# Performance work log

Hardware: AMD Instinct MI355X
Metric: run time of the kernel (lower is better)

The kernel has to match this reference:

```python
import jax, jax.numpy as jnp
import numpy as np

FG_THRESH = 0.5   # cfg.TRAIN.FG_THRESH
BG_THRESH = 0.1   # cfg.TRAIN.BG_THRESH
EPS = 1e-9
N_STREAMS = 4

def _area(b):
    return (b[..., 2] - b[..., 0] + 1.0) * (b[..., 3] - b[..., 1] + 1.0)

def _pairwise_iou(bb, gt):
    # bb [R,4], gt [G,4] -> [R,G] pascal IoU (with +1)
    x1 = jnp.maximum(bb[:, None, 0], gt[None, :, 0])
    y1 = jnp.maximum(bb[:, None, 1], gt[None, :, 1])
    x2 = jnp.minimum(bb[:, None, 2], gt[None, :, 2])
    y2 = jnp.minimum(bb[:, None, 3], gt[None, :, 3])
    iw = jnp.maximum(x2 - x1 + 1.0, 0.0)
    ih = jnp.maximum(y2 - y1 + 1.0, 0.0)
    inter = iw * ih
    return inter / (_area(bb)[:, None] + _area(gt)[None, :] - inter)

def _iou_vs_one(boxes, bm):
    # boxes [4,4] vs single box bm [4] -> mutual iou [4]
    x1 = jnp.maximum(boxes[:, 0], bm[0])
    y1 = jnp.maximum(boxes[:, 1], bm[1])
    x2 = jnp.minimum(boxes[:, 2], bm[2])
    y2 = jnp.minimum(boxes[:, 3], bm[3])
    iw = jnp.maximum(x2 - x1 + 1.0, 0.0)
    ih = jnp.maximum(y2 - y1 + 1.0, 0.0)
    inter = iw * ih
    return inter / (_area(boxes) + _area(bm) - inter)

def _select_per_class(boxes, present):
    # boxes [4,4] top proposals of the 4 streams for one class; present: bool
    # Faithful port of the instance_selector while-loop (at most 4 iterations).
    area = _area(boxes)
    active = jnp.full((N_STREAMS,), present)
    selected = jnp.zeros((N_STREAMS,), bool)
    idx = jnp.arange(N_STREAMS)
    for _ in range(N_STREAMS):
        m = jnp.argmax(jnp.where(active, area, -jnp.inf))
        bm = boxes[m]
        iou = _iou_vs_one(boxes, bm)
        enclosed = ((boxes[:, 0] > bm[0]) & (boxes[:, 1] > bm[1]) &
                    (boxes[:, 2] < bm[2]) & (boxes[:, 3] < bm[3]))
        pick = active & (idx == m)                      # max-area pick
        keep = active & (iou < 0.1) & (~enclosed)        # kept as extra gt
        selected = selected | pick | keep
        # removed: high-overlap (>0.3, includes m itself), enclosed, kept
        active = active & ~((iou > 0.3) | enclosed | keep)
    return selected

def instance_selector(cls_probs, rois, im_labels):
    # cls_probs [4,R,C], rois [R,4], im_labels [1,C]
    top_idx = jnp.argmax(cls_probs, axis=1)                      # [4,C]
    top_boxes = rois[top_idx]                                    # [4,C,4]
    top_scores = jnp.take_along_axis(cls_probs, top_idx[:, None, :], axis=1)[:, 0, :]  # [4,C]
    boxes_c = jnp.transpose(top_boxes, (1, 0, 2))                # [C,4,4]
    scores_c = top_scores.T                                      # [C,4]
    present = im_labels[0] > 0                                   # [C]
    selected = jax.vmap(_select_per_class)(boxes_c, present)     # [C,4]
    C = scores_c.shape[0]
    gt_boxes = boxes_c.reshape(-1, 4)                            # [4C,4]
    gt_scores = scores_c.reshape(-1)                             # [4C]
    gt_classes = jnp.repeat(jnp.arange(1, C + 1), N_STREAMS)     # [4C]
    return gt_boxes, gt_classes, gt_scores, selected.reshape(-1)

def pcl_loss(rois, cls_prob_new, gt_boxes, gt_classes, gt_scores, valid):
    R = rois.shape[0]
    G = gt_boxes.shape[0]
    ov = _pairwise_iou(rois, gt_boxes)                   # [R,G]
    ov = jnp.where(valid[None, :], ov, -1.0)             # mask unselected gts
    assign = jnp.argmax(ov, axis=1)
    maxov = jnp.max(ov, axis=1)
    lab = gt_classes[assign]
    w = gt_scores[assign]
    bg = maxov < FG_THRESH
    lab = jnp.where(bg, 0, lab)
    assign = jnp.where(bg, -1, assign)
    w = jnp.where(maxov < BG_THRESH, 0.0, w)
    p = jnp.clip(cls_prob_new, EPS, 1.0 - EPS)
    prob_a = p[jnp.arange(R), lab]                       # prob at assigned class
    fg = (assign >= 0).astype(p.dtype)
    seg = jnp.where(assign >= 0, assign, G)              # dummy bucket G
    sums = jax.ops.segment_sum(prob_a * fg, seg, num_segments=G + 1)[:G]
    counts = jax.ops.segment_sum(fg, seg, num_segments=G + 1)[:G]
    mean_prob = sums / jnp.maximum(counts, 1.0)
    mean_safe = jnp.where(counts > 0, mean_prob, 1.0)
    pos = -jnp.sum(jnp.where(valid & (counts > 0),
                             jnp.log(mean_safe) * counts * gt_scores, 0.0))
    n_mask = jnp.where(lab == 0, w, 0.0)
    neg = -jnp.sum(jnp.log(p[:, 0]) * n_mask)
    return (pos + neg) / max(800, R)

def setup_inputs() -> dict:
    key = jax.random.key(0)
    ks = jax.random.split(key, 10)
    R, C, W, H = 100000, 20, 1000.0, 1000.0
    cx = jax.random.uniform(ks[0], (R,)) * (W - 100.0) + 50.0
    cy = jax.random.uniform(ks[1], (R,)) * (H - 100.0) + 50.0
    bw = jax.random.uniform(ks[2], (R,)) * 400.0 + 16.0
    bh = jax.random.uniform(ks[3], (R,)) * 400.0 + 16.0
    x1 = jnp.clip(cx - bw / 2, 0.0, W - 2.0)
    y1 = jnp.clip(cy - bh / 2, 0.0, H - 2.0)
    x2 = jnp.maximum(jnp.minimum(cx + bw / 2, W - 1.0), x1 + 1.0)
    y2 = jnp.maximum(jnp.minimum(cy + bh / 2, H - 1.0), y1 + 1.0)
    rois = jnp.stack([x1, y1, x2, y2], axis=1).astype(jnp.float32)
    cls0 = jax.random.uniform(ks[4], (R, C), dtype=jnp.float32)
    cls1 = jax.random.uniform(ks[5], (R, C), dtype=jnp.float32)
    cls2 = jax.random.uniform(ks[6], (R, C), dtype=jnp.float32)
    cls3 = jax.random.uniform(ks[7], (R, C), dtype=jnp.float32)
    cls_prob_new = jax.nn.softmax(jax.random.normal(ks[8], (R, C + 1), dtype=jnp.float32), axis=1)
    im_labels = (jax.random.uniform(ks[9], (1, C)) < 0.15).astype(jnp.int32)
    im_labels = im_labels.at[0, 0].set(1)  # ensure at least one positive class
    return {"rois": rois, "cls0_prob": cls0, "cls1_prob": cls1,
            "cls2_prob": cls2, "cls3_prob": cls3,
            "cls_prob_new": cls_prob_new, "im_labels": im_labels}

def reference(rois, cls0_prob, cls1_prob, cls2_prob, cls3_prob, cls_prob_new, im_labels):
    cls_probs = jnp.stack([cls0_prob, cls1_prob, cls2_prob, cls3_prob])  # [4,R,C]
    gtb, gtc, gts, valid = instance_selector(cls_probs, rois, im_labels)
    loss = pcl_loss(rois, cls_prob_new, gtb, gtc, gts, valid)
    return loss, gtb, gts, valid
```

## Files before the change

kernel.cpp:

```cpp
#include <hip/hip_runtime.h>
#include <cfloat>
#include <climits>
#include <math.h>

#define NSTREAM 4
#define NCLS    20
#define NGT     (NSTREAM * NCLS)
#define NBLK    128
#define TPB     256

__global__ __launch_bounds__(TPB) void top_argmax_kernel(
    const float* __restrict__ c0, const float* __restrict__ c1,
    const float* __restrict__ c2, const float* __restrict__ c3,
    float* __restrict__ pv, int* __restrict__ pi, int R)
{
    const float* cls = (blockIdx.y == 0) ? c0 : (blockIdx.y == 1) ? c1
                     : (blockIdx.y == 2) ? c2 : c3;
    const int tid = threadIdx.x;
    const int gid = blockIdx.x * TPB + tid;
    const int stride = gridDim.x * TPB;

    float bv[NCLS];
    int   bi[NCLS];
#pragma unroll
    for (int c = 0; c < NCLS; ++c) { bv[c] = -FLT_MAX; bi[c] = 0; }

    for (int r = gid; r < R; r += stride) {
        const float4* row = reinterpret_cast<const float4*>(cls + (size_t)r * NCLS);
#pragma unroll
        for (int q = 0; q < NCLS / 4; ++q) {
            float4 v = row[q];
            float vals[4] = { v.x, v.y, v.z, v.w };
#pragma unroll
            for (int k = 0; k < 4; ++k) {
                const int c = q * 4 + k;
                if (vals[k] > bv[c]) { bv[c] = vals[k]; bi[c] = r; }
            }
        }
    }

    __shared__ float sv[NCLS][TPB];
    __shared__ int   si[NCLS][TPB];
#pragma unroll
    for (int c = 0; c < NCLS; ++c) { sv[c][tid] = bv[c]; si[c][tid] = bi[c]; }
    __syncthreads();

    for (int off = TPB / 2; off > 0; off >>= 1) {
        if (tid < off) {
#pragma unroll
            for (int c = 0; c < NCLS; ++c) {
                float ov = sv[c][tid + off]; int oi = si[c][tid + off];
                float mv = sv[c][tid];       int mi = si[c][tid];
                if (ov > mv || (ov == mv && oi < mi)) { sv[c][tid] = ov; si[c][tid] = oi; }
            }
        }
        __syncthreads();
    }

    if (tid < NCLS) {
        const int p = blockIdx.y * NCLS + tid;
        pv[(size_t)p * gridDim.x + blockIdx.x] = sv[tid][0];
        pi[(size_t)p * gridDim.x + blockIdx.x] = si[tid][0];
    }
}

__global__ __launch_bounds__(TPB) void select_kernel(
    const float* __restrict__ rois,
    const float* __restrict__ pv, const int* __restrict__ pi,
    const int* __restrict__ im_labels,
    float* __restrict__ ws_gtb, float* __restrict__ ws_gts,
    int* __restrict__ ws_valid,
    float* __restrict__ ws_sums, float* __restrict__ ws_cnts,
    float* __restrict__ ws_neg,
    float* __restrict__ d_out, int nblk)
{
    const int tid = threadIdx.x;
    __shared__ float s_box[NGT][4];

    if (tid < NGT) {
        const int s = tid / NCLS;
        const int c = tid % NCLS;
        const float* v  = pv + (size_t)tid * nblk;
        const int*   ii = pi + (size_t)tid * nblk;
        float best = -FLT_MAX; int bidx = INT_MAX;
        for (int b = 0; b < nblk; ++b) {
            float val = v[b]; int idx = ii[b];
            if (val > best || (val == best && idx < bidx)) { best = val; bidx = idx; }
        }
        const int g = c * NSTREAM + s;
        float4 box = reinterpret_cast<const float4*>(rois)[bidx];
        s_box[g][0] = box.x; s_box[g][1] = box.y; s_box[g][2] = box.z; s_box[g][3] = box.w;
        ws_gtb[g * 4 + 0] = box.x; ws_gtb[g * 4 + 1] = box.y;
        ws_gtb[g * 4 + 2] = box.z; ws_gtb[g * 4 + 3] = box.w;
        ws_gts[g] = best;
        d_out[1 + g * 4 + 0] = box.x; d_out[1 + g * 4 + 1] = box.y;
        d_out[1 + g * 4 + 2] = box.z; d_out[1 + g * 4 + 3] = box.w;
        d_out[1 + NGT * 4 + g] = best;
    }
    if (tid < NGT) { ws_sums[tid] = 0.0f; ws_cnts[tid] = 0.0f; }
    if (tid == 0)  { ws_neg[0] = 0.0f; }
    __syncthreads();

    if (tid < NCLS) {
        const int c = tid;
        const bool present = im_labels[c] > 0;
        float bx[NSTREAM][4], area[NSTREAM];
#pragma unroll
        for (int s = 0; s < NSTREAM; ++s) {
#pragma unroll
            for (int k = 0; k < 4; ++k) bx[s][k] = s_box[c * NSTREAM + s][k];
            area[s] = (bx[s][2] - bx[s][0] + 1.0f) * (bx[s][3] - bx[s][1] + 1.0f);
        }
        bool active[NSTREAM], sel[NSTREAM];
#pragma unroll
        for (int s = 0; s < NSTREAM; ++s) { active[s] = present; sel[s] = false; }

        for (int it = 0; it < NSTREAM; ++it) {
            int m = 0; float best = -FLT_MAX;
#pragma unroll
            for (int s = 0; s < NSTREAM; ++s) {
                float v = active[s] ? area[s] : -FLT_MAX;
                if (v > best) { best = v; m = s; }
            }
            const float bmx1 = bx[m][0], bmy1 = bx[m][1], bmx2 = bx[m][2], bmy2 = bx[m][3];
            const float am = area[m];
            bool nact[NSTREAM];
#pragma unroll
            for (int s = 0; s < NSTREAM; ++s) {
                float x1 = fmaxf(bx[s][0], bmx1), y1 = fmaxf(bx[s][1], bmy1);
                float x2 = fminf(bx[s][2], bmx2), y2 = fminf(bx[s][3], bmy2);
                float iw = fmaxf(x2 - x1 + 1.0f, 0.0f), ih = fmaxf(y2 - y1 + 1.0f, 0.0f);
                float inter = iw * ih;
                float iou = inter / (area[s] + am - inter);
                bool enclosed = (bx[s][0] > bmx1) && (bx[s][1] > bmy1) &&
                                (bx[s][2] < bmx2) && (bx[s][3] < bmy2);
                bool pick = active[s] && (s == m);
                bool keep = active[s] && (iou < 0.1f) && (!enclosed);
                sel[s] = sel[s] || pick || keep;
                nact[s] = active[s] && !((iou > 0.3f) || enclosed || keep);
            }
#pragma unroll
            for (int s = 0; s < NSTREAM; ++s) active[s] = nact[s];
        }
#pragma unroll
        for (int s = 0; s < NSTREAM; ++s) {
            const int g = c * NSTREAM + s;
            ws_valid[g] = sel[s] ? 1 : 0;
            d_out[1 + NGT * 4 + NGT + g] = sel[s] ? 1.0f : 0.0f;
        }
    }
}

__global__ __launch_bounds__(TPB) void assign_kernel(
    const float* __restrict__ rois, const float* __restrict__ clsnew,
    const float* __restrict__ ws_gtb, const float* __restrict__ ws_gts,
    const int* __restrict__ ws_valid,
    float* __restrict__ ws_sums, float* __restrict__ ws_cnts,
    float* __restrict__ ws_neg, int R)
{
    __shared__ float4 s_gt[NGT];
    __shared__ float  s_ga[NGT];
    __shared__ float  s_gs[NGT];
    __shared__ int    s_val[NGT];
    __shared__ float  s_sum[NGT];
    __shared__ float  s_cnt[NGT];
    __shared__ float  s_neg;

    const int tid = threadIdx.x;
    if (tid < NGT) {
        float4 b = reinterpret_cast<const float4*>(ws_gtb)[tid];
        s_gt[tid] = b;
        s_ga[tid] = (b.z - b.x + 1.0f) * (b.w - b.y + 1.0f);
        s_gs[tid] = ws_gts[tid];
        s_val[tid] = ws_valid[tid];
        s_sum[tid] = 0.0f; s_cnt[tid] = 0.0f;
    }
    if (tid == 0) s_neg = 0.0f;
    __syncthreads();

    const int r = blockIdx.x * TPB + tid;
    if (r < R) {
        float4 bb = reinterpret_cast<const float4*>(rois)[r];
        float ab = (bb.z - bb.x + 1.0f) * (bb.w - bb.y + 1.0f);
        float best = -FLT_MAX; int assign = 0;
        for (int g = 0; g < NGT; ++g) {
            float v;
            if (s_val[g]) {
                float4 gt = s_gt[g];
                float x1 = fmaxf(bb.x, gt.x), y1 = fmaxf(bb.y, gt.y);
                float x2 = fminf(bb.z, gt.z), y2 = fminf(bb.w, gt.w);
                float iw = fmaxf(x2 - x1 + 1.0f, 0.0f), ih = fmaxf(y2 - y1 + 1.0f, 0.0f);
                float inter = iw * ih;
                v = inter / (ab + s_ga[g] - inter);
            } else {
                v = -1.0f;
            }
            if (v > best) { best = v; assign = g; }
        }
        if (best >= 0.5f) {
            int lab = assign / NSTREAM + 1;
            float pa = clsnew[(size_t)r * (NCLS + 1) + lab];
            pa = fminf(fmaxf(pa, 1e-9f), 1.0f - 1e-9f);
            atomicAdd(&s_sum[assign], pa);
            atomicAdd(&s_cnt[assign], 1.0f);
        } else if (best >= 0.1f) {
            float p0 = clsnew[(size_t)r * (NCLS + 1)];
            p0 = fminf(fmaxf(p0, 1e-9f), 1.0f - 1e-9f);
            atomicAdd(&s_neg, logf(p0) * s_gs[assign]);
        }
    }
    __syncthreads();

    if (tid < NGT) {
        if (s_cnt[tid] != 0.0f) {
            atomicAdd(&ws_sums[tid], s_sum[tid]);
            atomicAdd(&ws_cnts[tid], s_cnt[tid]);
        }
    }
    if (tid == 0 && s_neg != 0.0f) atomicAdd(ws_neg, s_neg);
}

__global__ __launch_bounds__(128) void finalize_kernel(
    const float* __restrict__ ws_sums, const float* __restrict__ ws_cnts,
    const float* __restrict__ ws_gts, const int* __restrict__ ws_valid,
    const float* __restrict__ ws_neg, float* __restrict__ d_out, int R)
{
    __shared__ float red[128];
    const int tid = threadIdx.x;
    float t = 0.0f;
    if (tid < NGT) {
        float cnt = ws_cnts[tid];
        if (ws_valid[tid] && cnt > 0.0f) {
            float mean = ws_sums[tid] / fmaxf(cnt, 1.0f);
            t = logf(mean) * cnt * ws_gts[tid];
        }
    }
    red[tid] = t;
    __syncthreads();
    for (int off = 64; off > 0; off >>= 1) {
        if (tid < off) red[tid] += red[tid + off];
        __syncthreads();
    }
    if (tid == 0) {
        float pos = -red[0];
        float neg = -ws_neg[0];
        float denom = fmaxf(800.0f, (float)R);
        d_out[0] = (pos + neg) / denom;
    }
}

extern "C" void kernel_launch(void* const* d_in, const int* in_sizes, int n_in,
                              void* d_out, int out_size, void* d_ws, size_t ws_size,
                              hipStream_t stream) {
    const float* rois   = (const float*)d_in[0];
    const float* c0     = (const float*)d_in[1];
    const float* c1     = (const float*)d_in[2];
    const float* c2     = (const float*)d_in[3];
    const float* c3     = (const float*)d_in[4];
    const float* clsnew = (const float*)d_in[5];
    const int*   imlab  = (const int*)d_in[6];
    const int R = in_sizes[0] / 4;

    float* ws    = (float*)d_ws;
    float* pv    = ws;
    int*   pi    = (int*)(pv + NSTREAM * NCLS * NBLK);
    float* gtb   = (float*)(pi + NSTREAM * NCLS * NBLK);
    float* gts   = gtb + NGT * 4;
    int*   valid = (int*)(gts + NGT);
    float* sums  = (float*)(valid + NGT);
    float* cnts  = sums + NGT;
    float* neg   = cnts + NGT;

    float* out = (float*)d_out;

    dim3 gridA(NBLK, NSTREAM);
    top_argmax_kernel<<<gridA, TPB, 0, stream>>>(c0, c1, c2, c3, pv, pi, R);
    select_kernel<<<1, TPB, 0, stream>>>(rois, pv, pi, imlab, gtb, gts, valid,
                                         sums, cnts, neg, out, NBLK);
    assign_kernel<<<(R + TPB - 1) / TPB, TPB, 0, stream>>>(rois, clsnew, gtb, gts,
                                                           valid, sums, cnts, neg, R);
    finalize_kernel<<<1, 128, 0, stream>>>(sums, cnts, gts, valid, neg, out, R);
}
```

Measured before the change: 154.9 us.

## Fuse four kernels into one cooperative kernel with grid syncs

Replaces the four separate launches (argmax, select, assign, finalize) with a single cooperative kernel of 512 blocks that uses grid.sync between phases, cutting launch gaps. The block-level argmax reduction now uses wavefront shuffles instead of a large shared-memory tree. The assign phase iterates only over a compacted list of valid GT boxes and uses a grid-stride loop. The trade-off is the cost of grid-wide barriers, and the requirement that all blocks be co-resident.

```diff
diff --git a/kernel.cpp b/kernel.cpp
--- a/kernel.cpp
+++ b/kernel.cpp
@@ -1,251 +1,267 @@
 #include <hip/hip_runtime.h>
+#include <hip/hip_cooperative_groups.h>
 #include <cfloat>
 #include <climits>
 #include <math.h>
 
+namespace cg = cooperative_groups;
+
 #define NSTREAM 4
 #define NCLS    20
 #define NGT     (NSTREAM * NCLS)
-#define NBLK    128
+#define XBLK    128
+#define GRID    (XBLK * NSTREAM)
 #define TPB     256
 
-__global__ __launch_bounds__(TPB) void top_argmax_kernel(
+
+__global__ __launch_bounds__(TPB) void fused_kernel(
+    const float* __restrict__ rois,
     const float* __restrict__ c0, const float* __restrict__ c1,
     const float* __restrict__ c2, const float* __restrict__ c3,
-    float* __restrict__ pv, int* __restrict__ pi, int R)
+    const float* __restrict__ clsnew,
+    const int* __restrict__ imlab,
+    float* ws, float* __restrict__ d_out, int R)
 {
-    const float* cls = (blockIdx.y == 0) ? c0 : (blockIdx.y == 1) ? c1
-                     : (blockIdx.y == 2) ? c2 : c3;
-    const int tid = threadIdx.x;
-    const int gid = blockIdx.x * TPB + tid;
-    const int stride = gridDim.x * TPB;
-
-    float bv[NCLS];
-    int   bi[NCLS];
-#pragma unroll
-    for (int c = 0; c < NCLS; ++c) { bv[c] = -FLT_MAX; bi[c] = 0; }
-
-    for (int r = gid; r < R; r += stride) {
-        const float4* row = reinterpret_cast<const float4*>(cls + (size_t)r * NCLS);
-#pragma unroll
-        for (int q = 0; q < NCLS / 4; ++q) {
-            float4 v = row[q];
-            float vals[4] = { v.x, v.y, v.z, v.w };
-#pragma unroll
-            for (int k = 0; k < 4; ++k) {
-                const int c = q * 4 + k;
-                if (vals[k] > bv[c]) { bv[c] = vals[k]; bi[c] = r; }
-            }
-        }
-    }
-
-    __shared__ float sv[NCLS][TPB];
-    __shared__ int   si[NCLS][TPB];
-#pragma unroll
-    for (int c = 0; c < NCLS; ++c) { sv[c][tid] = bv[c]; si[c][tid] = bi[c]; }
-    __syncthreads();
-
-    for (int off = TPB / 2; off > 0; off >>= 1) {
-        if (tid < off) {
-#pragma unroll
-            for (int c = 0; c < NCLS; ++c) {
-                float ov = sv[c][tid + off]; int oi = si[c][tid + off];
-                float mv = sv[c][tid];       int mi = si[c][tid];
-                if (ov > mv || (ov == mv && oi < mi)) { sv[c][tid] = ov; si[c][tid] = oi; }
-            }
-        }
-        __syncthreads();
-    }
-
-    if (tid < NCLS) {
-        const int p = blockIdx.y * NCLS + tid;
-        pv[(size_t)p * gridDim.x + blockIdx.x] = sv[tid][0];
-        pi[(size_t)p * gridDim.x + blockIdx.x] = si[tid][0];
-    }
-}
-
-__global__ __launch_bounds__(TPB) void select_kernel(
-    const float* __restrict__ rois,
-    const float* __restrict__ pv, const int* __restrict__ pi,
-    const int* __restrict__ im_labels,
-    float* __restrict__ ws_gtb, float* __restrict__ ws_gts,
-    int* __restrict__ ws_valid,
-    float* __restrict__ ws_sums, float* __restrict__ ws_cnts,
-    float* __restrict__ ws_neg,
-    float* __restrict__ d_out, int nblk)
-{
-    const int tid = threadIdx.x;
+    cg::grid_group grid = cg::this_grid();
+
+    float* pv    = ws;
+    int*   pi    = (int*)(ws + 10240);
+    float* gtb   = ws + 20480;
+    float* gts   = ws + 20800;
+    int*   valid = (int*)(ws + 20880);
+    float* sums  = ws + 20960;
+    float* cnts  = ws + 21040;
+    float* negp  = ws + 21120;
+    int*   nvp   = (int*)(ws + 21121);
+    int*   glist = (int*)(ws + 21122);
+
+    const int bid  = blockIdx.x;
+    const int tid  = threadIdx.x;
+    const int lane = tid & 63;
+    const int wv   = tid >> 6;
+
+    __shared__ float sv[NCLS][4];
+    __shared__ int   si[NCLS][4];
     __shared__ float s_box[NGT][4];
-
-    if (tid < NGT) {
-        const int s = tid / NCLS;
-        const int c = tid % NCLS;
-        const float* v  = pv + (size_t)tid * nblk;
-        const int*   ii = pi + (size_t)tid * nblk;
-        float best = -FLT_MAX; int bidx = INT_MAX;
-        for (int b = 0; b < nblk; ++b) {
-            float val = v[b]; int idx = ii[b];
-            if (val > best || (val == best && idx < bidx)) { best = val; bidx = idx; }
-        }
-        const int g = c * NSTREAM + s;
-        float4 box = reinterpret_cast<const float4*>(rois)[bidx];
-        s_box[g][0] = box.x; s_box[g][1] = box.y; s_box[g][2] = box.z; s_box[g][3] = box.w;
-        ws_gtb[g * 4 + 0] = box.x; ws_gtb[g * 4 + 1] = box.y;
-        ws_gtb[g * 4 + 2] = box.z; ws_gtb[g * 4 + 3] = box.w;
-        ws_gts[g] = best;
-        d_out[1 + g * 4 + 0] = box.x; d_out[1 + g * 4 + 1] = box.y;
-        d_out[1 + g * 4 + 2] = box.z; d_out[1 + g * 4 + 3] = box.w;
-        d_out[1 + NGT * 4 + g] = best;
-    }
-    if (tid < NGT) { ws_sums[tid] = 0.0f; ws_cnts[tid] = 0.0f; }
-    if (tid == 0)  { ws_neg[0] = 0.0f; }
-    __syncthreads();
-
-    if (tid < NCLS) {
-        const int c = tid;
-        const bool present = im_labels[c] > 0;
-        float bx[NSTREAM][4], area[NSTREAM];
-#pragma unroll
-        for (int s = 0; s < NSTREAM; ++s) {
-#pragma unroll
-            for (int k = 0; k < 4; ++k) bx[s][k] = s_box[c * NSTREAM + s][k];
-            area[s] = (bx[s][2] - bx[s][0] + 1.0f) * (bx[s][3] - bx[s][1] + 1.0f);
-        }
-        bool active[NSTREAM], sel[NSTREAM];
-#pragma unroll
-        for (int s = 0; s < NSTREAM; ++s) { active[s] = present; sel[s] = false; }
-
-        for (int it = 0; it < NSTREAM; ++it) {
-            int m = 0; float best = -FLT_MAX;
-#pragma unroll
-            for (int s = 0; s < NSTREAM; ++s) {
-                float v = active[s] ? area[s] : -FLT_MAX;
-                if (v > best) { best = v; m = s; }
-            }
-            const float bmx1 = bx[m][0], bmy1 = bx[m][1], bmx2 = bx[m][2], bmy2 = bx[m][3];
-            const float am = area[m];
-            bool nact[NSTREAM];
-#pragma unroll
-            for (int s = 0; s < NSTREAM; ++s) {
-                float x1 = fmaxf(bx[s][0], bmx1), y1 = fmaxf(bx[s][1], bmy1);
-                float x2 = fminf(bx[s][2], bmx2), y2 = fminf(bx[s][3], bmy2);
-                float iw = fmaxf(x2 - x1 + 1.0f, 0.0f), ih = fmaxf(y2 - y1 + 1.0f, 0.0f);
-                float inter = iw * ih;
-                float iou = inter / (area[s] + am - inter);
-                bool enclosed = (bx[s][0] > bmx1) && (bx[s][1] > bmy1) &&
-                                (bx[s][2] < bmx2) && (bx[s][3] < bmy2);
-                bool pick = active[s] && (s == m);
-                bool keep = active[s] && (iou < 0.1f) && (!enclosed);
-                sel[s] = sel[s] || pick || keep;
-                nact[s] = active[s] && !((iou > 0.3f) || enclosed || keep);
-            }
-#pragma unroll
-            for (int s = 0; s < NSTREAM; ++s) active[s] = nact[s];
-        }
-#pragma unroll
-        for (int s = 0; s < NSTREAM; ++s) {
-            const int g = c * NSTREAM + s;
-            ws_valid[g] = sel[s] ? 1 : 0;
-            d_out[1 + NGT * 4 + NGT + g] = sel[s] ? 1.0f : 0.0f;
-        }
-    }
-}
-
-__global__ __launch_bounds__(TPB) void assign_kernel(
-    const float* __restrict__ rois, const float* __restrict__ clsnew,
-    const float* __restrict__ ws_gtb, const float* __restrict__ ws_gts,
-    const int* __restrict__ ws_valid,
-    float* __restrict__ ws_sums, float* __restrict__ ws_cnts,
-    float* __restrict__ ws_neg, int R)
-{
     __shared__ float4 s_gt[NGT];
     __shared__ float  s_ga[NGT];
     __shared__ float  s_gs[NGT];
-    __shared__ int    s_val[NGT];
+    __shared__ int    s_lab[NGT];
+    __shared__ int    s_gidx[NGT];
     __shared__ float  s_sum[NGT];
     __shared__ float  s_cnt[NGT];
     __shared__ float  s_neg;
-
-    const int tid = threadIdx.x;
-    if (tid < NGT) {
-        float4 b = reinterpret_cast<const float4*>(ws_gtb)[tid];
-        s_gt[tid] = b;
-        s_ga[tid] = (b.z - b.x + 1.0f) * (b.w - b.y + 1.0f);
-        s_gs[tid] = ws_gts[tid];
-        s_val[tid] = ws_valid[tid];
-        s_sum[tid] = 0.0f; s_cnt[tid] = 0.0f;
-    }
-    if (tid == 0) s_neg = 0.0f;
-    __syncthreads();
-
-    const int r = blockIdx.x * TPB + tid;
-    if (r < R) {
-        float4 bb = reinterpret_cast<const float4*>(rois)[r];
-        float ab = (bb.z - bb.x + 1.0f) * (bb.w - bb.y + 1.0f);
-        float best = -FLT_MAX; int assign = 0;
-        for (int g = 0; g < NGT; ++g) {
-            float v;
-            if (s_val[g]) {
-                float4 gt = s_gt[g];
+    __shared__ float  s_wred[4];
+
+    {
+        const int s  = bid >> 7;
+        const int xb = bid & (XBLK - 1);
+        const float* cls = (s == 0) ? c0 : (s == 1) ? c1 : (s == 2) ? c2 : c3;
+
+        float bv[NCLS];
+        int   bi_[NCLS];
+#pragma unroll
+        for (int c = 0; c < NCLS; ++c) { bv[c] = -FLT_MAX; bi_[c] = 0; }
+
+        const int gid = xb * TPB + tid;
+        const int stride = XBLK * TPB;
+        for (int r = gid; r < R; r += stride) {
+            const float4* row = reinterpret_cast<const float4*>(cls + (size_t)r * NCLS);
+#pragma unroll
+            for (int q = 0; q < NCLS / 4; ++q) {
+                float4 v = row[q];
+                float vals[4] = { v.x, v.y, v.z, v.w };
+#pragma unroll
+                for (int k = 0; k < 4; ++k) {
+                    const int c = q * 4 + k;
+                    if (vals[k] > bv[c]) { bv[c] = vals[k]; bi_[c] = r; }
+                }
+            }
+        }
+#pragma unroll
+        for (int off = 32; off > 0; off >>= 1) {
+#pragma unroll
+            for (int c = 0; c < NCLS; ++c) {
+                float ov = __shfl_down(bv[c], off);
+                int   oi = __shfl_down(bi_[c], off);
+                if (ov > bv[c] || (ov == bv[c] && oi < bi_[c])) { bv[c] = ov; bi_[c] = oi; }
+            }
+        }
+        if (lane == 0) {
+#pragma unroll
+            for (int c = 0; c < NCLS; ++c) { sv[c][wv] = bv[c]; si[c][wv] = bi_[c]; }
+        }
+        __syncthreads();
+        if (tid < NCLS) {
+            float best = sv[tid][0]; int bidx = si[tid][0];
+#pragma unroll
+            for (int w = 1; w < 4; ++w) {
+                float v = sv[tid][w]; int i = si[tid][w];
+                if (v > best || (v == best && i < bidx)) { best = v; bidx = i; }
+            }
+            const int p = s * NCLS + tid;
+            pv[(size_t)p * XBLK + xb] = best;
+            pi[(size_t)p * XBLK + xb] = bidx;
+        }
+    }
+
+    grid.sync();
+
+    if (bid == 0) {
+        if (tid < NGT) {
+            const int st = tid / NCLS;
+            const int c  = tid % NCLS;
+            const float* v  = pv + (size_t)tid * XBLK;
+            const int*   ii = pi + (size_t)tid * XBLK;
+            float best = -FLT_MAX; int bidx = INT_MAX;
+            for (int b = 0; b < XBLK; ++b) {
+                float val = v[b]; int idx = ii[b];
+                if (val > best || (val == best && idx < bidx)) { best = val; bidx = idx; }
+            }
+            const int g = c * NSTREAM + st;
+            float4 box = reinterpret_cast<const float4*>(rois)[bidx];
+            s_box[g][0] = box.x; s_box[g][1] = box.y;
+            s_box[g][2] = box.z; s_box[g][3] = box.w;
+            gtb[g * 4 + 0] = box.x; gtb[g * 4 + 1] = box.y;
+            gtb[g * 4 + 2] = box.z; gtb[g * 4 + 3] = box.w;
+            gts[g] = best;
+            d_out[1 + g * 4 + 0] = box.x; d_out[1 + g * 4 + 1] = box.y;
+            d_out[1 + g * 4 + 2] = box.z; d_out[1 + g * 4 + 3] = box.w;
+            d_out[1 + NGT * 4 + g] = best;
+            sums[g] = 0.0f; cnts[g] = 0.0f;
+        }
+        if (tid == 0) negp[0] = 0.0f;
+        __syncthreads();
+
+        if (tid < NCLS) {
+            const int c = tid;
+            const bool present = imlab[c] > 0;
+            float bx[NSTREAM][4], area[NSTREAM];
+#pragma unroll
+            for (int s = 0; s < NSTREAM; ++s) {
+#pragma unroll
+                for (int k = 0; k < 4; ++k) bx[s][k] = s_box[c * NSTREAM + s][k];
+                area[s] = (bx[s][2] - bx[s][0] + 1.0f) * (bx[s][3] - bx[s][1] + 1.0f);
+            }
+            bool active[NSTREAM], sel[NSTREAM];
+#pragma unroll
+            for (int s = 0; s < NSTREAM; ++s) { active[s] = present; sel[s] = false; }
+
+            for (int it = 0; it < NSTREAM; ++it) {
+                int m = 0; float best = -FLT_MAX;
+#pragma unroll
+                for (int s = 0; s < NSTREAM; ++s) {
+                    float v = active[s] ? area[s] : -FLT_MAX;
+                    if (v > best) { best = v; m = s; }
+                }
+                const float bmx1 = bx[m][0], bmy1 = bx[m][1];
+                const float bmx2 = bx[m][2], bmy2 = bx[m][3];
+                const float am = area[m];
+                bool nact[NSTREAM];
+#pragma unroll
+                for (int s = 0; s < NSTREAM; ++s) {
+                    float x1 = fmaxf(bx[s][0], bmx1), y1 = fmaxf(bx[s][1], bmy1);
+                    float x2 = fminf(bx[s][2], bmx2), y2 = fminf(bx[s][3], bmy2);
+                    float iw = fmaxf(x2 - x1 + 1.0f, 0.0f), ih = fmaxf(y2 - y1 + 1.0f, 0.0f);
+                    float inter = iw * ih;
+                    float iou = inter / (area[s] + am - inter);
+                    bool enclosed = (bx[s][0] > bmx1) && (bx[s][1] > bmy1) &&
+                                    (bx[s][2] < bmx2) && (bx[s][3] < bmy2);
+                    bool pick = active[s] && (s == m);
+                    bool keep = active[s] && (iou < 0.1f) && (!enclosed);
+                    sel[s] = sel[s] || pick || keep;
+                    nact[s] = active[s] && !((iou > 0.3f) || enclosed || keep);
+                }
+#pragma unroll
+                for (int s = 0; s < NSTREAM; ++s) active[s] = nact[s];
+            }
+#pragma unroll
+            for (int s = 0; s < NSTREAM; ++s) {
+                const int g = c * NSTREAM + s;
+                valid[g] = sel[s] ? 1 : 0;
+                d_out[1 + NGT * 4 + NGT + g] = sel[s] ? 1.0f : 0.0f;
+            }
+        }
+        __syncthreads();
+
+        if (tid == 0) {
+            int nv = 0;
+            for (int g = 0; g < NGT; ++g) if (valid[g]) glist[nv++] = g;
+            nvp[0] = nv;
+        }
+    }
+
+    grid.sync();
+
+    {
+        const int nv = nvp[0];
+        if (tid < nv) {
+            const int g = glist[tid];
+            float4 b = reinterpret_cast<const float4*>(gtb)[g];
+            s_gt[tid] = b;
+            s_ga[tid] = (b.z - b.x + 1.0f) * (b.w - b.y + 1.0f);
+            s_gs[tid] = gts[g];
+            s_lab[tid] = g / NSTREAM + 1;
+            s_gidx[tid] = g;
+        }
+        if (tid < NGT) { s_sum[tid] = 0.0f; s_cnt[tid] = 0.0f; }
+        if (tid == 0) s_neg = 0.0f;
+        __syncthreads();
+
+        for (int r = bid * TPB + tid; r < R; r += GRID * TPB) {
+            float4 bb = reinterpret_cast<const float4*>(rois)[r];
+            float ab = (bb.z - bb.x + 1.0f) * (bb.w - bb.y + 1.0f);
+            float best = -FLT_MAX; int bestj = 0;
+            for (int j = 0; j < nv; ++j) {
+                float4 gt = s_gt[j];
                 float x1 = fmaxf(bb.x, gt.x), y1 = fmaxf(bb.y, gt.y);
                 float x2 = fminf(bb.z, gt.z), y2 = fminf(bb.w, gt.w);
                 float iw = fmaxf(x2 - x1 + 1.0f, 0.0f), ih = fmaxf(y2 - y1 + 1.0f, 0.0f);
                 float inter = iw * ih;
-                v = inter / (ab + s_ga[g] - inter);
-            } else {
-                v = -1.0f;
-            }
-            if (v > best) { best = v; assign = g; }
-        }
-        if (best >= 0.5f) {
-            int lab = assign / NSTREAM + 1;
-            float pa = clsnew[(size_t)r * (NCLS + 1) + lab];
-            pa = fminf(fmaxf(pa, 1e-9f), 1.0f - 1e-9f);
-            atomicAdd(&s_sum[assign], pa);
-            atomicAdd(&s_cnt[assign], 1.0f);
-        } else if (best >= 0.1f) {
-            float p0 = clsnew[(size_t)r * (NCLS + 1)];
-            p0 = fminf(fmaxf(p0, 1e-9f), 1.0f - 1e-9f);
-            atomicAdd(&s_neg, logf(p0) * s_gs[assign]);
-        }
-    }
-    __syncthreads();
-
-    if (tid < NGT) {
-        if (s_cnt[tid] != 0.0f) {
-            atomicAdd(&ws_sums[tid], s_sum[tid]);
-            atomicAdd(&ws_cnts[tid], s_cnt[tid]);
-        }
-    }
-    if (tid == 0 && s_neg != 0.0f) atomicAdd(ws_neg, s_neg);
-}
-
-__global__ __launch_bounds__(128) void finalize_kernel(
-    const float* __restrict__ ws_sums, const float* __restrict__ ws_cnts,
-    const float* __restrict__ ws_gts, const int* __restrict__ ws_valid,
-    const float* __restrict__ ws_neg, float* __restrict__ d_out, int R)
-{
-    __shared__ float red[128];
-    const int tid = threadIdx.x;
-    float t = 0.0f;
-    if (tid < NGT) {
-        float cnt = ws_cnts[tid];
-        if (ws_valid[tid] && cnt > 0.0f) {
-            float mean = ws_sums[tid] / fmaxf(cnt, 1.0f);
-            t = logf(mean) * cnt * ws_gts[tid];
-        }
-    }
-    red[tid] = t;
-    __syncthreads();
-    for (int off = 64; off > 0; off >>= 1) {
-        if (tid < off) red[tid] += red[tid + off];
-        __syncthreads();
-    }
-    if (tid == 0) {
-        float pos = -red[0];
-        float neg = -ws_neg[0];
-        float denom = fmaxf(800.0f, (float)R);
-        d_out[0] = (pos + neg) / denom;
+                float v = inter / (ab + s_ga[j] - inter);
+                if (v > best) { best = v; bestj = j; }
+            }
+            if (nv > 0) {
+                if (best >= 0.5f) {
+                    const int lab = s_lab[bestj];
+                    float pa = clsnew[(size_t)r * (NCLS + 1) + lab];
+                    pa = fminf(fmaxf(pa, 1e-9f), 1.0f - 1e-9f);
+                    atomicAdd(&s_sum[bestj], pa);
+                    atomicAdd(&s_cnt[bestj], 1.0f);
+                } else if (best >= 0.1f) {
+                    float p0 = clsnew[(size_t)r * (NCLS + 1)];
+                    p0 = fminf(fmaxf(p0, 1e-9f), 1.0f - 1e-9f);
+                    atomicAdd(&s_neg, logf(p0) * s_gs[bestj]);
+                }
+            }
+        }
+        __syncthreads();
+
+        if (tid < nv && s_cnt[tid] != 0.0f) {
+            atomicAdd(&sums[s_gidx[tid]], s_sum[tid]);
+            atomicAdd(&cnts[s_gidx[tid]], s_cnt[tid]);
+        }
+        if (tid == 0 && s_neg != 0.0f) atomicAdd(negp, s_neg);
+    }
+
+    grid.sync();
+
+    if (bid == 0) {
+        float t = 0.0f;
+        if (tid < NGT) {
+            float cnt = cnts[tid];
+            if (valid[tid] && cnt > 0.0f)
+                t = logf(sums[tid] / cnt) * cnt * gts[tid];
+        }
+#pragma unroll
+        for (int off = 32; off > 0; off >>= 1) t += __shfl_down(t, off);
+        if (lane == 0) s_wred[wv] = t;
+        __syncthreads();
+        if (tid == 0) {
+            float pos = -(s_wred[0] + s_wred[1] + s_wred[2] + s_wred[3]);
+            float neg = -negp[0];
+            d_out[0] = (pos + neg) / fmaxf(800.0f, (float)R);
+        }
     }
 }
 
@@ -259,25 +275,13 @@
     const float* c3     = (const float*)d_in[4];
     const float* clsnew = (const float*)d_in[5];
     const int*   imlab  = (const int*)d_in[6];
-    const int R = in_sizes[0] / 4;
-
-    float* ws    = (float*)d_ws;
-    float* pv    = ws;
-    int*   pi    = (int*)(pv + NSTREAM * NCLS * NBLK);
-    float* gtb   = (float*)(pi + NSTREAM * NCLS * NBLK);
-    float* gts   = gtb + NGT * 4;
-    int*   valid = (int*)(gts + NGT);
-    float* sums  = (float*)(valid + NGT);
-    float* cnts  = sums + NGT;
-    float* neg   = cnts + NGT;
-
+    int R = in_sizes[0] / 4;
+
+    float* ws  = (float*)d_ws;
     float* out = (float*)d_out;
 
-    dim3 gridA(NBLK, NSTREAM);
-    top_argmax_kernel<<<gridA, TPB, 0, stream>>>(c0, c1, c2, c3, pv, pi, R);
-    select_kernel<<<1, TPB, 0, stream>>>(rois, pv, pi, imlab, gtb, gts, valid,
-                                         sums, cnts, neg, out, NBLK);
-    assign_kernel<<<(R + TPB - 1) / TPB, TPB, 0, stream>>>(rois, clsnew, gtb, gts,
-                                                           valid, sums, cnts, neg, R);
-    finalize_kernel<<<1, 128, 0, stream>>>(sums, cnts, gts, valid, neg, out, R);
+    void* args[] = { (void*)&rois, (void*)&c0, (void*)&c1, (void*)&c2, (void*)&c3,
+                     (void*)&clsnew, (void*)&imlab, (void*)&ws, (void*)&out, (void*)&R };
+    hipLaunchCooperativeKernel((const void*)fused_kernel, dim3(GRID), dim3(TPB),
+                               args, 0, stream);
 }
```

Result: slower. 322.3 us (+108.1%).
